# Optimization experiments

Measured on AMD Instinct MI355X. Metric: run time of the kernel, lower is better.

The kernel has to match this reference:

```python
import jax, jax.numpy as jnp
import numpy as np

B, S, HID = 2, 2048, 2048
H = 16
NOPE, ROPE, V_DIM, KV_RANK = 128, 64, 128, 512
Q_DIM = NOPE + ROPE  # 192
EPS = 1e-6
NEG = -1e9


def setup_inputs() -> dict:
    key = jax.random.key(0)
    ks = jax.random.split(key, 5)
    return {
        "hidden_states": jax.random.normal(ks[0], (B, S, HID), jnp.float32),
        "q_proj_w": jax.random.normal(ks[1], (H * Q_DIM, HID), jnp.float32) * (HID ** -0.5),
        "kv_a_proj_w": jax.random.normal(ks[2], (KV_RANK + ROPE, HID), jnp.float32) * (HID ** -0.5),
        "kv_a_ln_w": jnp.ones((KV_RANK,), jnp.float32),
        "kv_b_proj_w": jax.random.normal(ks[3], (H * (NOPE + V_DIM), KV_RANK), jnp.float32) * (KV_RANK ** -0.5),
        "o_proj_w": jax.random.normal(ks[4], (HID, H * V_DIM), jnp.float32) * ((H * V_DIM) ** -0.5),
    }


def _rmsnorm(x, w):
    xf = x.astype(jnp.float32)
    var = jnp.mean(xf * xf, axis=-1, keepdims=True)
    return (w * (xf * jax.lax.rsqrt(var + EPS)).astype(x.dtype))


def reference(hidden_states, q_proj_w, kv_a_proj_w, kv_a_ln_w, kv_b_proj_w, o_proj_w):
    b, s, _ = hidden_states.shape
    scaling = Q_DIM ** -0.5

    # query projection -> [b, h, s, q_dim]
    q = (hidden_states @ q_proj_w.T).reshape(b, s, H, Q_DIM).transpose(0, 2, 1, 3)

    # latent kv projection
    compressed = hidden_states @ kv_a_proj_w.T            # [b, s, kv_rank+rope]
    k_pass_lat = compressed[..., :KV_RANK]                # [b, s, kv_rank]
    k_rot = compressed[..., KV_RANK:]                     # [b, s, rope]

    kv = (_rmsnorm(k_pass_lat, kv_a_ln_w) @ kv_b_proj_w.T)  # [b, s, h*(nope+v)]
    kv = kv.reshape(b, s, H, NOPE + V_DIM).transpose(0, 2, 1, 3)  # [b, h, s, nope+v]
    k_pass = kv[..., :NOPE]                               # [b, h, s, nope]
    v = kv[..., NOPE:]                                    # [b, h, s, v]

    k_rot = jnp.broadcast_to(k_rot[:, None, :, :], (b, H, s, ROPE))
    k = jnp.concatenate([k_pass, k_rot], axis=-1)         # [b, h, s, q_dim]

    # causal attention (eager path), softmax in fp32
    scores = jnp.einsum("bhqd,bhkd->bhqk", q, k) * scaling
    causal = jnp.tril(jnp.ones((s, s), bool))
    scores = jnp.where(causal[None, None], scores, NEG)
    probs = jax.nn.softmax(scores.astype(jnp.float32), axis=-1).astype(q.dtype)

    out = jnp.einsum("bhqk,bhkd->bhqd", probs, v)         # [b, h, s, v]
    out = out.transpose(0, 2, 1, 3).reshape(b, s, H * V_DIM)
    return out @ o_proj_w.T
```

## Files before the change

kernel.cpp:

```cpp
#include <hip/hip_runtime.h>
#include <stdint.h>
#include <stddef.h>

#define B_    2
#define S_    2048
#define HID_  2048
#define H_    16
#define NOPE_ 128
#define ROPE_ 64
#define VD_   128
#define RANK_ 512
#define QD_   192
#define M_    4096
#define NEGV  (-1e9f)

typedef __attribute__((ext_vector_type(8))) __bf16 bf16x8;
typedef __attribute__((ext_vector_type(8))) short  short8;
typedef __attribute__((ext_vector_type(4))) short  short4v;
typedef __attribute__((ext_vector_type(4))) float  f32x4;

__device__ __forceinline__ short f2bf(float f) {
  uint32_t u = __builtin_bit_cast(uint32_t, f);
  u += 0x7fffu + ((u >> 16) & 1u);
  return (short)(u >> 16);
}

__device__ __forceinline__ void gll16(const void* g, void* l) {
  __builtin_amdgcn_global_load_lds(
      (__attribute__((address_space(1))) void*)(g),
      (__attribute__((address_space(3))) void*)(l), 16, 0, 0);
}

__device__ __forceinline__ f32x4 mfma16(short8 a, short8 b, f32x4 c) {
  return __builtin_amdgcn_mfma_f32_16x16x32_bf16(
      __builtin_bit_cast(bf16x8, a), __builtin_bit_cast(bf16x8, b), c, 0, 0, 0);
}

__global__ void k_cast4(const float* __restrict__ in, short* __restrict__ out, int n4) {
  int i = blockIdx.x * blockDim.x + threadIdx.x;
  if (i >= n4) return;
  float4 v = *(const float4*)(in + (size_t)i * 4);
  short4v o = { f2bf(v.x), f2bf(v.y), f2bf(v.z), f2bf(v.w) };
  *(short4v*)(out + (size_t)i * 4) = o;
}

__global__ void k_cast_kva(const float* __restrict__ in, short* __restrict__ out) {
  int i = blockIdx.x * blockDim.x + threadIdx.x;
  int e = i * 4;
  int r = e >> 11, c = e & 2047;
  short4v o = {0, 0, 0, 0};
  if (r < 576) {
    float4 v = *(const float4*)(in + (size_t)r * 2048 + c);
    o[0] = f2bf(v.x); o[1] = f2bf(v.y); o[2] = f2bf(v.z); o[3] = f2bf(v.w);
  }
  *(short4v*)(out + e) = o;
}

template <typename OutT>
__global__ __launch_bounds__(256) void k_gemm_bt(
    const short* __restrict__ A, const short* __restrict__ Bm,
    OutT* __restrict__ C, int M, int N, int K)
{
  __shared__ __align__(16) short As[128 * 64];
  __shared__ __align__(16) short Bs[128 * 64];
  const int tid = threadIdx.x;
  const int lane = tid & 63, wid = tid >> 6;
  const int l15 = lane & 15, lhi = lane >> 4;
  const int brow = blockIdx.y * 128, bcol = blockIdx.x * 128;
  const int wr = (wid >> 1) * 64, wc = (wid & 1) * 64;

  f32x4 acc[4][4];
#pragma unroll
  for (int i = 0; i < 4; ++i)
#pragma unroll
    for (int j = 0; j < 4; ++j) acc[i][j] = (f32x4)0.f;

  const int srow = lane >> 3;
  const int scol = ((lane & 7) ^ srow) * 8;

  for (int k0 = 0; k0 < K; k0 += 64) {
    __syncthreads();
#pragma unroll
    for (int i = 0; i < 4; ++i) {
      int seg = wid * 4 + i;
      int row = seg * 8 + srow;
      gll16(A  + (size_t)(brow + row) * K + k0 + scol, &As[seg * 512]);
      gll16(Bm + (size_t)(bcol + row) * K + k0 + scol, &Bs[seg * 512]);
    }
    __syncthreads();
#pragma unroll
    for (int ks = 0; ks < 2; ++ks) {
      short8 af[4], bfr[4];
#pragma unroll
      for (int i = 0; i < 4; ++i) {
        int r = wr + i * 16 + l15;
        af[i] = *(const short8*)&As[r * 64 + (((ks * 4 + lhi) ^ (l15 & 7)) << 3)];
      }
#pragma unroll
      for (int j = 0; j < 4; ++j) {
        int r = wc + j * 16 + l15;
        bfr[j] = *(const short8*)&Bs[r * 64 + (((ks * 4 + lhi) ^ (l15 & 7)) << 3)];
      }
#pragma unroll
      for (int i = 0; i < 4; ++i)
#pragma unroll
        for (int j = 0; j < 4; ++j) acc[i][j] = mfma16(af[i], bfr[j], acc[i][j]);
    }
  }
#pragma unroll
  for (int i = 0; i < 4; ++i) {
    int r0 = brow + wr + i * 16 + lhi * 4;
#pragma unroll
    for (int j = 0; j < 4; ++j) {
      int c = bcol + wc + j * 16 + l15;
#pragma unroll
      for (int t = 0; t < 4; ++t) {
        float v = acc[i][j][t];
        if constexpr (__is_same(OutT, float)) C[(size_t)(r0 + t) * N + c] = v;
        else                                  C[(size_t)(r0 + t) * N + c] = f2bf(v);
      }
    }
  }
}

__global__ __launch_bounds__(256) void k_rms(
    const float* __restrict__ comp,
    const float* __restrict__ w,
    short* __restrict__ normed,
    short* __restrict__ krot)
{
  __shared__ float red[4];
  const int row = blockIdx.x, tid = threadIdx.x;
  const float* x = comp + (size_t)row * 640;
  float v0 = x[tid], v1 = x[tid + 256];
  float ss = v0 * v0 + v1 * v1;
#pragma unroll
  for (int off = 1; off < 64; off <<= 1) ss += __shfl_xor(ss, off);
  if ((tid & 63) == 0) red[tid >> 6] = ss;
  __syncthreads();
  float rs = rsqrtf((red[0] + red[1] + red[2] + red[3]) * (1.f / 512.f) + 1e-6f);
  normed[(size_t)row * 512 + tid]       = f2bf(w[tid] * v0 * rs);
  normed[(size_t)row * 512 + tid + 256] = f2bf(w[tid + 256] * v1 * rs);
  if (tid < 64) krot[(size_t)row * 64 + tid] = f2bf(x[512 + tid]);
}

__global__ __launch_bounds__(256) void k_vtrans(
    const short* __restrict__ kv, short* __restrict__ vt)
{
  __shared__ __align__(16) short t[64][136];
  const int tid = threadIdx.x;
  const int st = blockIdx.x, bh = blockIdx.y;
  const int b = bh >> 4, h = bh & 15;
  const int s0 = st * 64;
#pragma unroll
  for (int i = 0; i < 4; ++i) {
    int e8 = i * 256 + tid;
    int r = e8 >> 4, c = (e8 & 15) * 8;
    short8 v = *(const short8*)&kv[(size_t)(b * S_ + s0 + r) * 4096 + h * 256 + 128 + c];
    *(short8*)&t[r][c] = v;
  }
  __syncthreads();
#pragma unroll
  for (int i = 0; i < 4; ++i) {
    int e8 = i * 256 + tid;
    int d = e8 >> 3, sc = (e8 & 7) * 8;
    short8 o;
#pragma unroll
    for (int k = 0; k < 8; ++k) o[k] = t[sc + k][d];
    *(short8*)&vt[((size_t)bh * 128 + d) * S_ + s0 + sc] = o;
  }
}

__global__ __launch_bounds__(512) void k_attn(
    const short* __restrict__ q,
    const short* __restrict__ kv,
    const short* __restrict__ krot,
    const short* __restrict__ vt,
    short* __restrict__ outp)
{
  __shared__ __align__(16) short Kp[64 * 128];
  __shared__ __align__(16) short Kr[64 * 64];
  __shared__ __align__(16) short Vt[128 * 64];
  __shared__ __align__(16) short Ps[128 * 64];

  const int tid = threadIdx.x, lane = tid & 63, wid = tid >> 6;
  const int l15 = lane & 15, lhi = lane >> 4;
  const int o = blockIdx.x;
  const int w = (o & 7) * 64 + (o >> 3);
  const int bh = w >> 4;
  const int qtb = 15 - (w & 15);
  const int b = bh >> 4, h = bh & 15;
  const int q0 = qtb * 128;
  const int ktmax = 2 * qtb + 1;

  const int sr8 = lane >> 3;
  const int sc8 = ((lane & 7) ^ sr8) * 8;

  short8 qf[6];
  {
    const short* qp = q + (size_t)(b * S_ + q0 + wid * 16 + l15) * (H_ * QD_) + h * QD_ + lhi * 8;
#pragma unroll
    for (int ks = 0; ks < 6; ++ks) qf[ks] = *(const short8*)(qp + ks * 32);
  }

  float m_run[4] = {-1e30f, -1e30f, -1e30f, -1e30f};
  float l_run[4] = {0.f, 0.f, 0.f, 0.f};
  f32x4 oa[8];
#pragma unroll
  for (int j = 0; j < 8; ++j) oa[j] = (f32x4)0.f;

  const float scale = 0.07216878f;

  for (int kt = 0; kt <= ktmax; ++kt) {
    const int krow0 = b * S_ + kt * 64;
    __syncthreads();
#pragma unroll
    for (int i = 0; i < 2; ++i) {
      int seg = wid * 2 + i;
      int row = seg * 4 + (lane >> 4);
      int col = ((lane & 15) ^ (row & 7)) * 8;
      gll16(kv + (size_t)(krow0 + row) * 4096 + h * 256 + col, &Kp[seg * 512]);
    }
    {
      int seg = wid;
      int row = seg * 8 + sr8;
      gll16(krot + (size_t)(krow0 + row) * 64 + sc8, &Kr[seg * 512]);
    }
#pragma unroll
    for (int i = 0; i < 2; ++i) {
      int seg = wid * 2 + i;
      int d = seg * 8 + sr8;
      gll16(vt + ((size_t)bh * 128 + d) * S_ + kt * 64 + sc8, &Vt[seg * 512]);
    }
    __syncthreads();

    const bool active = (kt * 64) <= (q0 + wid * 16 + 15);

    if (active) {
      f32x4 sf[4];
#pragma unroll
      for (int fc = 0; fc < 4; ++fc) sf[fc] = (f32x4)0.f;
#pragma unroll
      for (int fc = 0; fc < 4; ++fc) {
        int n = fc * 16 + l15, nx = n & 7;
#pragma unroll
        for (int ks = 0; ks < 4; ++ks) {
          short8 kf = *(const short8*)&Kp[n * 128 + (((ks * 4 + lhi) ^ nx) << 3)];
          sf[fc] = mfma16(qf[ks], kf, sf[fc]);
        }
#pragma unroll
        for (int ks = 4; ks < 6; ++ks) {
          short8 kf = *(const short8*)&Kr[n * 64 + ((((ks - 4) * 4 + lhi) ^ nx) << 3)];
          sf[fc] = mfma16(qf[ks], kf, sf[fc]);
        }
      }
      if (kt * 64 + 63 > q0 + wid * 16) {
#pragma unroll
        for (int fc = 0; fc < 4; ++fc) {
          int kl = kt * 64 + fc * 16 + l15;
#pragma unroll
          for (int r = 0; r < 4; ++r) {
            int ql = q0 + wid * 16 + lhi * 4 + r;
            sf[fc][r] = (kl <= ql) ? sf[fc][r] * scale : NEGV;
          }
        }
      } else {
#pragma unroll
        for (int fc = 0; fc < 4; ++fc)
#pragma unroll
          for (int r = 0; r < 4; ++r) sf[fc][r] *= scale;
      }
      float mnew[4], scf[4], rsum[4];
#pragma unroll
      for (int r = 0; r < 4; ++r) {
        float t = fmaxf(fmaxf(sf[0][r], sf[1][r]), fmaxf(sf[2][r], sf[3][r]));
#pragma unroll
        for (int off = 1; off < 16; off <<= 1) t = fmaxf(t, __shfl_xor(t, off));
        mnew[r] = fmaxf(m_run[r], t);
        scf[r] = __expf(m_run[r] - mnew[r]);
        m_run[r] = mnew[r];
        rsum[r] = 0.f;
      }
#pragma unroll
      for (int fc = 0; fc < 4; ++fc)
#pragma unroll
        for (int r = 0; r < 4; ++r) {
          float p = __expf(sf[fc][r] - mnew[r]);
          sf[fc][r] = p;
          rsum[r] += p;
        }
#pragma unroll
      for (int r = 0; r < 4; ++r) {
        float t = rsum[r];
#pragma unroll
        for (int off = 1; off < 16; off <<= 1) t += __shfl_xor(t, off);
        l_run[r] = l_run[r] * scf[r] + t;
      }
#pragma unroll
      for (int j = 0; j < 8; ++j)
#pragma unroll
        for (int r = 0; r < 4; ++r) oa[j][r] *= scf[r];
#pragma unroll
      for (int fc = 0; fc < 4; ++fc)
#pragma unroll
        for (int r = 0; r < 4; ++r) {
          int pr = wid * 16 + lhi * 4 + r;
          int pc = fc * 16 + l15;
          Ps[pr * 64 + ((((pc >> 3) ^ (pr & 7)) << 3) | (pc & 7))] = f2bf(sf[fc][r]);
        }
    }
    __syncthreads();
    if (active) {
      short8 pa[2];
      {
        int prow = wid * 16 + l15, px = prow & 7;
#pragma unroll
        for (int ks = 0; ks < 2; ++ks)
          pa[ks] = *(const short8*)&Ps[prow * 64 + (((ks * 4 + lhi) ^ px) << 3)];
      }
#pragma unroll
      for (int j = 0; j < 8; ++j) {
        int d = j * 16 + l15, dx = d & 7;
#pragma unroll
        for (int ks = 0; ks < 2; ++ks) {
          short8 vb = *(const short8*)&Vt[d * 64 + (((ks * 4 + lhi) ^ dx) << 3)];
          oa[j] = mfma16(pa[ks], vb, oa[j]);
        }
      }
    }
  }
#pragma unroll
  for (int j = 0; j < 8; ++j)
#pragma unroll
    for (int r = 0; r < 4; ++r) {
      size_t row = (size_t)(b * S_ + q0 + wid * 16 + lhi * 4 + r);
      int col = h * 128 + j * 16 + l15;
      outp[row * 2048 + col] = f2bf(oa[j][r] / l_run[r]);
    }
}

extern "C" void kernel_launch(void* const* d_in, const int* in_sizes, int n_in,
                              void* d_out, int out_size, void* d_ws, size_t ws_size,
                              hipStream_t stream) {
  const float* hidden = (const float*)d_in[0];
  const float* qw     = (const float*)d_in[1];
  const float* kvaw   = (const float*)d_in[2];
  const float* lnw    = (const float*)d_in[3];
  const float* kvbw   = (const float*)d_in[4];
  const float* ow     = (const float*)d_in[5];

  char* ws = (char*)d_ws;
  short* hidb  = (short*)(ws + 0);
  short* qwb   = (short*)(ws + 16777216);
  short* kvawb = (short*)(ws + 29360128);
  short* kvbwb = (short*)(ws + 31981568);
  short* owb   = (short*)(ws + 36175872);
  short* qb    = (short*)(ws + 44564480);
  float* comp  = (float*)(ws + 69730304);
  short* normb = (short*)(ws + 80216064);
  short* krotb = (short*)(ws + 84410368);
  short* kvb   = (short*)(ws + 84934656);
  short* vtb   = (short*)(ws + 118489088);
  short* attnb = (short*)(ws + 135266304);

  k_cast4<<<8192, 256, 0, stream>>>(hidden, hidb, 2097152);
  k_cast4<<<6144, 256, 0, stream>>>(qw, qwb, 1572864);
  k_cast_kva<<<1280, 256, 0, stream>>>(kvaw, kvawb);
  k_cast4<<<2048, 256, 0, stream>>>(kvbw, kvbwb, 524288);
  k_cast4<<<4096, 256, 0, stream>>>(ow, owb, 1048576);

  k_gemm_bt<short><<<dim3(24, 32), 256, 0, stream>>>(hidb, qwb, qb, M_, 3072, 2048);
  k_gemm_bt<float><<<dim3(5, 32), 256, 0, stream>>>(hidb, kvawb, comp, M_, 640, 2048);
  k_rms<<<4096, 256, 0, stream>>>(comp, lnw, normb, krotb);
  k_gemm_bt<short><<<dim3(32, 32), 256, 0, stream>>>(normb, kvbwb, kvb, M_, 4096, 512);
  k_vtrans<<<dim3(32, 32), 256, 0, stream>>>(kvb, vtb);

  k_attn<<<512, 512, 0, stream>>>(qb, kvb, krotb, vtb, attnb);

  k_gemm_bt<float><<<dim3(16, 32), 256, 0, stream>>>(attnb, owb, (float*)d_out, M_, 2048, 2048);
}
```

Before: 485.6 us.

## Prefetch next K/V tile into registers and drop per-wave P barrier

Replaces direct global-to-LDS loads of the K, K-rope and V tiles with a register prefetch. The next tile's loads are issued right after the current tile is written to LDS, so global latency overlaps with the QK, softmax and PV compute. The block-wide barrier between writing P and reading it is replaced by an LDS waitcnt, since each wave only reads its own P rows. It also sets launch_bounds min-waves to 4, which raises register pressure and risks spills given the extra prefetch registers.

```diff
diff --git a/kernel.cpp b/kernel.cpp
--- a/kernel.cpp
+++ b/kernel.cpp
@@ -171,7 +171,7 @@
   }
 }
 
-__global__ __launch_bounds__(512) void k_attn(
+__global__ __launch_bounds__(512, 4) void k_attn(
     const short* __restrict__ q,
     const short* __restrict__ kv,
     const short* __restrict__ krot,
@@ -196,6 +196,31 @@
   const int sr8 = lane >> 3;
   const int sc8 = ((lane & 7) ^ sr8) * 8;
 
+  short8 rKp0, rKp1, rKr, rVt0, rVt1;
+  const int kpRow  = wid * 8 + (lane >> 4);
+  const int kpCol0 = ((lane & 15) ^ (kpRow & 7)) * 8;
+  const int kpRow1 = kpRow + 4;
+  const int kpCol1 = ((lane & 15) ^ (kpRow1 & 7)) * 8;
+  const int krRow  = wid * 8 + sr8;
+  const int vtD0   = wid * 16 + sr8;
+  const int vtD1   = vtD0 + 8;
+
+  auto LOADR = [&](int kt) {
+    const int krow0 = b * S_ + kt * 64;
+    rKp0 = *(const short8*)(kv + (size_t)(krow0 + kpRow) * 4096 + h * 256 + kpCol0);
+    rKp1 = *(const short8*)(kv + (size_t)(krow0 + kpRow1) * 4096 + h * 256 + kpCol1);
+    rKr  = *(const short8*)(krot + (size_t)(krow0 + krRow) * 64 + sc8);
+    rVt0 = *(const short8*)(vt + ((size_t)bh * 128 + vtD0) * S_ + kt * 64 + sc8);
+    rVt1 = *(const short8*)(vt + ((size_t)bh * 128 + vtD1) * S_ + kt * 64 + sc8);
+  };
+  auto WRITES = [&]() {
+    *(short8*)&Kp[(wid * 2) * 512 + lane * 8]     = rKp0;
+    *(short8*)&Kp[(wid * 2 + 1) * 512 + lane * 8] = rKp1;
+    *(short8*)&Kr[wid * 512 + lane * 8]           = rKr;
+    *(short8*)&Vt[(wid * 2) * 512 + lane * 8]     = rVt0;
+    *(short8*)&Vt[(wid * 2 + 1) * 512 + lane * 8] = rVt1;
+  };
+
   short8 qf[6];
   {
     const short* qp = q + (size_t)(b * S_ + q0 + wid * 16 + l15) * (H_ * QD_) + h * QD_ + lhi * 8;
@@ -211,28 +236,15 @@
 
   const float scale = 0.07216878f;
 
+  LOADR(0);
+
   for (int kt = 0; kt <= ktmax; ++kt) {
-    const int krow0 = b * S_ + kt * 64;
     __syncthreads();
-#pragma unroll
-    for (int i = 0; i < 2; ++i) {
-      int seg = wid * 2 + i;
-      int row = seg * 4 + (lane >> 4);
-      int col = ((lane & 15) ^ (row & 7)) * 8;
-      gll16(kv + (size_t)(krow0 + row) * 4096 + h * 256 + col, &Kp[seg * 512]);
-    }
-    {
-      int seg = wid;
-      int row = seg * 8 + sr8;
-      gll16(krot + (size_t)(krow0 + row) * 64 + sc8, &Kr[seg * 512]);
-    }
-#pragma unroll
-    for (int i = 0; i < 2; ++i) {
-      int seg = wid * 2 + i;
-      int d = seg * 8 + sr8;
-      gll16(vt + ((size_t)bh * 128 + d) * S_ + kt * 64 + sc8, &Vt[seg * 512]);
-    }
-    __syncthreads();
+    WRITES();
+    asm volatile("s_waitcnt lgkmcnt(0)" ::: "memory");
+    if (kt < ktmax) LOADR(kt + 1);
+    __builtin_amdgcn_s_barrier();
+    __builtin_amdgcn_sched_barrier(0);
 
     const bool active = (kt * 64) <= (q0 + wid * 16 + 15);
 
@@ -308,9 +320,8 @@
           int pc = fc * 16 + l15;
           Ps[pr * 64 + ((((pc >> 3) ^ (pr & 7)) << 3) | (pc & 7))] = f2bf(sf[fc][r]);
         }
-    }
-    __syncthreads();
-    if (active) {
+      asm volatile("s_waitcnt lgkmcnt(0)" ::: "memory");
+      __builtin_amdgcn_sched_barrier(0);
       short8 pa[2];
       {
         int prow = wid * 16 + l15, px = prow & 7;
```

New measurement: 729.2 us. +50.2%, slower.
